# Kernel optimization log

Measured on AMD Instinct MI355X. Metric: run time of the kernel, lower is better.

Reference implementation:

```python
import jax, jax.numpy as jnp
import numpy as np

B, P, NEG = 1024, 10, 990
NU, NI = 10000, 20000
MOMENTUM = 0.9
EPS = 1e-10
FAIR_W = 100000.0


def setup_inputs() -> dict:
    key = jax.random.key(0)
    k1, k2, k3, k4, k5, k6 = jax.random.split(key, 6)
    predictions = jax.random.normal(k1, (B, P + NEG), dtype=jnp.float32)
    stats = jax.random.uniform(k2, (NU + 1, NI + 1), dtype=jnp.float32) * 0.1
    user_id = jax.random.randint(k3, (B,), 0, NU + 1)
    item_id = jax.random.randint(k4, (B, P), 0, NI + 1)
    # binary group indicator masks (float, as they multiply the softmax)
    a_index = (jax.random.uniform(k5, (B, P + NEG)) < 0.5).astype(jnp.float32)
    b_index = (jax.random.uniform(k6, (B, P + NEG)) < 0.5).astype(jnp.float32)
    return {"predictions": predictions, "stats": stats, "user_id": user_id,
            "item_id": item_id, "a_index": a_index, "b_index": b_index}


def reference(predictions, stats, user_id, item_id, a_index, b_index):
    batch_size = predictions.shape[0]
    # (batch pos) 1  and  (batch pos) neg
    pos = predictions[:, :P].reshape(batch_size * P, 1)
    neg = jnp.repeat(predictions[:, P:], P, axis=0)          # [(B*P), NEG]
    score_margins = neg - pos                                 # [(B*P), NEG]
    exp_margins = jax.lax.stop_gradient(
        jnp.exp(score_margins - jnp.max(score_margins)))
    user_rep = jnp.repeat(user_id, P)                         # [(B*P)]
    pos_items = item_id[:, :P].reshape(-1)                    # [(B*P)]
    exp_margin_means = jnp.mean(exp_margins, axis=1)
    current = stats[user_rep, pos_items]                      # gather
    updated = (1.0 - MOMENTUM) * current + MOMENTUM * exp_margin_means
    new_stats = stats.at[user_rep, pos_items].set(updated)    # scatter
    normalized = jax.lax.stop_gradient(exp_margins / (updated[:, None] + EPS))
    main_loss = jnp.sum(score_margins * normalized) / batch_size
    # fairness term (expectation_mode='1' -> unit expectation weights)
    psm = jax.nn.softmax(predictions, axis=1)
    a_exp = jnp.sum(a_index * psm, axis=1)
    b_exp = jnp.sum(b_index * psm, axis=1)
    diff = b_exp - a_exp
    fw_sqrt = np.sqrt(FAIR_W).astype(np.float32)
    fairness = (diff * fw_sqrt) ** 2                          # balanced
    loss = main_loss + jnp.mean(fairness)
    return loss, new_stats
```

## Files before the change

### kernel.cpp

```cpp
#include <hip/hip_runtime.h>
#include <math.h>

constexpr int kB    = 1024;
constexpr int kP    = 10;
constexpr int kNeg  = 990;
constexpr int kCols = 1000;
constexpr int kNI1  = 20001;
constexpr long long kStatsN = 200030001LL;
constexpr float kMom = 0.9f;
constexpr float kEps = 1e-10f;

constexpr int kOffT0   = 0;
constexpr int kOffT1   = 1024;
constexpr int kOffMM   = 2048;
constexpr int kOffFair = 3072;
constexpr int kOffM    = 4096;
constexpr int kOffFS   = 4097;
constexpr int kOffAcc  = 4098;
constexpr int kOffUpd  = 4100;
constexpr int kOffKey  = 14340;

__device__ inline float wave_sum(float v) {
    for (int o = 32; o > 0; o >>= 1) v += __shfl_xor(v, o, 64);
    return v;
}
__device__ inline float wave_max(float v) {
    for (int o = 32; o > 0; o >>= 1) v = fmaxf(v, __shfl_xor(v, o, 64));
    return v;
}
__device__ inline float wave_min(float v) {
    for (int o = 32; o > 0; o >>= 1) v = fminf(v, __shfl_xor(v, o, 64));
    return v;
}

__global__ __launch_bounds__(256) void k_rowstats(const float* __restrict__ pred,
                                                  const float* __restrict__ aidx,
                                                  const float* __restrict__ bidx,
                                                  float* __restrict__ ws) {
    const int b = blockIdx.x;
    const int t = threadIdx.x;
    const float* row = pred + (long long)b * kCols;
    const float* ar  = aidx + (long long)b * kCols;
    const float* br  = bidx + (long long)b * kCols;

    float sumexp = 0.f, sa = 0.f, sb = 0.f, T0 = 0.f, T1 = 0.f;
    float posmin = INFINITY, negmax = -INFINITY;
#pragma unroll
    for (int q = 0; q < 4; ++q) {
        int i = t + q * 256;
        if (i < kCols) {
            float x  = row[i];
            float ex = expf(x);
            sumexp += ex;
            sa += ar[i] * ex;
            sb += br[i] * ex;
            if (i < kP) {
                posmin = fminf(posmin, x);
            } else {
                negmax = fmaxf(negmax, x);
                T0 += ex;
                T1 += x * ex;
            }
        }
    }
    sumexp = wave_sum(sumexp);
    sa     = wave_sum(sa);
    sb     = wave_sum(sb);
    T0     = wave_sum(T0);
    T1     = wave_sum(T1);
    posmin = wave_min(posmin);
    negmax = wave_max(negmax);

    __shared__ float red[7][4];
    const int w = t >> 6, lane = t & 63;
    if (lane == 0) {
        red[0][w] = sumexp; red[1][w] = sa; red[2][w] = sb;
        red[3][w] = T0;     red[4][w] = T1;
        red[5][w] = posmin; red[6][w] = negmax;
    }
    __syncthreads();
    if (t == 0) {
        float se = 0.f, a = 0.f, bb = 0.f, t0 = 0.f, t1 = 0.f;
        float pm = INFINITY, nm = -INFINITY;
#pragma unroll
        for (int i = 0; i < 4; ++i) {
            se += red[0][i]; a += red[1][i]; bb += red[2][i];
            t0 += red[3][i]; t1 += red[4][i];
            pm = fminf(pm, red[5][i]); nm = fmaxf(nm, red[6][i]);
        }
        float diff = (bb - a) / se;
        float fw   = sqrtf(100000.0f);
        float d2   = diff * fw;
        ws[kOffT0 + b]   = t0;
        ws[kOffT1 + b]   = t1;
        ws[kOffMM + b]   = nm - pm;
        ws[kOffFair + b] = d2 * d2;
    }
}

__global__ __launch_bounds__(256) void k_reduce(float* __restrict__ ws) {
    const int t = threadIdx.x;
    float mm = -INFINITY, fs = 0.f;
#pragma unroll
    for (int q = 0; q < 4; ++q) {
        int i = t + q * 256;
        mm = fmaxf(mm, ws[kOffMM + i]);
        fs += ws[kOffFair + i];
    }
    mm = wave_max(mm);
    fs = wave_sum(fs);
    __shared__ float rm[4], rs[4];
    const int w = t >> 6, lane = t & 63;
    if (lane == 0) { rm[w] = mm; rs[w] = fs; }
    __syncthreads();
    if (t == 0) {
        float M = fmaxf(fmaxf(rm[0], rm[1]), fmaxf(rm[2], rm[3]));
        float F = rs[0] + rs[1] + rs[2] + rs[3];
        ws[kOffM]   = M;
        ws[kOffFS]  = F;
        ws[kOffAcc] = 0.f;
    }
}

__global__ __launch_bounds__(256) void k_perk(const float* __restrict__ pred,
                                              const float* __restrict__ stats,
                                              const int* __restrict__ uid,
                                              const int* __restrict__ iid,
                                              float* __restrict__ ws) {
    const int k = blockIdx.x * 256 + threadIdx.x;
    const float M = ws[kOffM];
    const int b = k / kP;
    const int p = k - b * kP;
    float pos = pred[(long long)b * kCols + p];
    float T0  = ws[kOffT0 + b];
    float T1  = ws[kOffT1 + b];
    float s   = expf(-pos - M);
    float mean_e = s * T0 * (1.0f / kNeg);
    int u  = uid[b];
    int it = iid[k];
    int key = u * kNI1 + it;
    float cur = stats[(long long)key];
    float upd = (1.0f - kMom) * cur + kMom * mean_e;
    ws[kOffUpd + k] = upd;
    ((int*)ws)[kOffKey + k] = key;
    float c = s * (T1 - pos * T0) / (upd + kEps);

    c = wave_sum(c);
    __shared__ float rs[4];
    const int w = threadIdx.x >> 6, lane = threadIdx.x & 63;
    if (lane == 0) rs[w] = c;
    __syncthreads();
    if (threadIdx.x == 0) {
        atomicAdd(&ws[kOffAcc], rs[0] + rs[1] + rs[2] + rs[3]);
    }
}

__global__ __launch_bounds__(256) void k_copy(const float* __restrict__ src,
                                              float* __restrict__ dst) {
    const long long base = (long long)blockIdx.x * 1024 + threadIdx.x;
#pragma unroll
    for (int q = 0; q < 4; ++q) {
        long long i = base + (long long)q * 256;
        if (i < kStatsN) dst[i] = src[i];
    }
}

__global__ __launch_bounds__(256) void k_scatter(float* __restrict__ out,
                                                 const float* __restrict__ ws) {
    const int k = blockIdx.x;
    const int* keys = (const int*)ws + kOffKey;
    __shared__ int dupflag;
    if (threadIdx.x == 0) dupflag = 0;
    __syncthreads();
    const int key = keys[k];
    for (int j = k + 1 + threadIdx.x; j < kB * kP; j += 256) {
        if (keys[j] == key) dupflag = 1;
    }
    __syncthreads();
    if (threadIdx.x == 0 && !dupflag) {
        out[1 + (long long)key] = ws[kOffUpd + k];
    }
    if (blockIdx.x == 0 && threadIdx.x == 255) {
        out[0] = ws[kOffAcc] * (1.0f / kB) + ws[kOffFS] * (1.0f / kB);
    }
}

extern "C" void kernel_launch(void* const* d_in, const int* in_sizes, int n_in,
                              void* d_out, int out_size, void* d_ws, size_t ws_size,
                              hipStream_t stream) {
    const float* pred  = (const float*)d_in[0];
    const float* stats = (const float*)d_in[1];
    const int*   uid   = (const int*)d_in[2];
    const int*   iid   = (const int*)d_in[3];
    const float* aidx  = (const float*)d_in[4];
    const float* bidx  = (const float*)d_in[5];
    float* out = (float*)d_out;
    float* ws  = (float*)d_ws;

    k_rowstats<<<kB, 256, 0, stream>>>(pred, aidx, bidx, ws);
    k_reduce<<<1, 256, 0, stream>>>(ws);
    k_perk<<<(kB * kP) / 256, 256, 0, stream>>>(pred, stats, uid, iid, ws);
    long long nblocks = (kStatsN + 1023) / 1024;
    k_copy<<<(int)nblocks, 256, 0, stream>>>(stats, out + 1);
    k_scatter<<<kB * kP, 256, 0, stream>>>(out, ws);
}
```

Measured before the change: 1.315 ms.

## Fuse stats copy into rowstats kernel and fold global reduce into perk

Merges the row-statistics kernel and the stats copy into one launch, with extra blocks that copy the stats table. Because the output is offset by one float, each block does float4 loads and shifts lanes so its stores are aligned, and a few edge elements are written separately. The separate single-block reduce kernel is removed: every perk block recomputes the global max margin, and block 0 writes the fairness sum. This saves launches and makes the large copy vectorised, at the cost of redundant reductions and two float4 loads per copied chunk.

After: 1.272 ms. 3.3% less time.

```diff
diff --git a/kernel.cpp b/kernel.cpp
--- a/kernel.cpp
+++ b/kernel.cpp
@@ -14,12 +14,16 @@
 constexpr int kOffT1   = 1024;
 constexpr int kOffMM   = 2048;
 constexpr int kOffFair = 3072;
-constexpr int kOffM    = 4096;
 constexpr int kOffFS   = 4097;
 constexpr int kOffAcc  = 4098;
 constexpr int kOffUpd  = 4100;
 constexpr int kOffKey  = 14340;
 
+constexpr long long kChunks = (kStatsN - 3) / 4;
+constexpr int kChunksPerBlock = 1024;
+constexpr int kCopyBlocks =
+    (int)((kChunks + kChunksPerBlock - 1) / kChunksPerBlock);
+
 __device__ inline float wave_sum(float v) {
     for (int o = 32; o > 0; o >>= 1) v += __shfl_xor(v, o, 64);
     return v;
@@ -33,92 +37,99 @@
     return v;
 }
 
-__global__ __launch_bounds__(256) void k_rowstats(const float* __restrict__ pred,
-                                                  const float* __restrict__ aidx,
-                                                  const float* __restrict__ bidx,
-                                                  float* __restrict__ ws) {
-    const int b = blockIdx.x;
+__global__ __launch_bounds__(256) void k_main(const float* __restrict__ pred,
+                                              const float* __restrict__ aidx,
+                                              const float* __restrict__ bidx,
+                                              const float* __restrict__ stats,
+                                              float* __restrict__ out,
+                                              float* __restrict__ ws) {
+    const int blk = blockIdx.x;
     const int t = threadIdx.x;
-    const float* row = pred + (long long)b * kCols;
-    const float* ar  = aidx + (long long)b * kCols;
-    const float* br  = bidx + (long long)b * kCols;
-
-    float sumexp = 0.f, sa = 0.f, sb = 0.f, T0 = 0.f, T1 = 0.f;
-    float posmin = INFINITY, negmax = -INFINITY;
+
+    if (blk < kB) {
+        if (blk == 0) {
+            if (t == 64) {
+                out[1] = stats[0]; out[2] = stats[1]; out[3] = stats[2];
+            } else if (t == 65) {
+                out[kStatsN - 1] = stats[kStatsN - 2];
+                out[kStatsN]     = stats[kStatsN - 1];
+            } else if (t == 66) {
+                ws[kOffAcc] = 0.f;
+            }
+        }
+        const int b = blk;
+        const float* row = pred + (long long)b * kCols;
+        const float* ar  = aidx + (long long)b * kCols;
+        const float* br  = bidx + (long long)b * kCols;
+
+        float sumexp = 0.f, sa = 0.f, sb = 0.f, T0 = 0.f, T1 = 0.f;
+        float posmin = INFINITY, negmax = -INFINITY;
+#pragma unroll
+        for (int q = 0; q < 4; ++q) {
+            int i = t + q * 256;
+            if (i < kCols) {
+                float x  = row[i];
+                float ex = expf(x);
+                sumexp += ex;
+                sa += ar[i] * ex;
+                sb += br[i] * ex;
+                if (i < kP) {
+                    posmin = fminf(posmin, x);
+                } else {
+                    negmax = fmaxf(negmax, x);
+                    T0 += ex;
+                    T1 += x * ex;
+                }
+            }
+        }
+        sumexp = wave_sum(sumexp);
+        sa     = wave_sum(sa);
+        sb     = wave_sum(sb);
+        T0     = wave_sum(T0);
+        T1     = wave_sum(T1);
+        posmin = wave_min(posmin);
+        negmax = wave_max(negmax);
+
+        __shared__ float red[7][4];
+        const int w = t >> 6, lane = t & 63;
+        if (lane == 0) {
+            red[0][w] = sumexp; red[1][w] = sa; red[2][w] = sb;
+            red[3][w] = T0;     red[4][w] = T1;
+            red[5][w] = posmin; red[6][w] = negmax;
+        }
+        __syncthreads();
+        if (t == 0) {
+            float se = 0.f, a = 0.f, bb = 0.f, t0 = 0.f, t1 = 0.f;
+            float pm = INFINITY, nm = -INFINITY;
+#pragma unroll
+            for (int i = 0; i < 4; ++i) {
+                se += red[0][i]; a += red[1][i]; bb += red[2][i];
+                t0 += red[3][i]; t1 += red[4][i];
+                pm = fminf(pm, red[5][i]); nm = fmaxf(nm, red[6][i]);
+            }
+            float diff = (bb - a) / se;
+            float fw   = sqrtf(100000.0f);
+            float d2   = diff * fw;
+            ws[kOffT0 + b]   = t0;
+            ws[kOffT1 + b]   = t1;
+            ws[kOffMM + b]   = nm - pm;
+            ws[kOffFair + b] = d2 * d2;
+        }
+        return;
+    }
+
+    const long long c0 = (long long)(blk - kB) * kChunksPerBlock + t;
+    const float4* __restrict__ s4 = (const float4*)stats;
 #pragma unroll
     for (int q = 0; q < 4; ++q) {
-        int i = t + q * 256;
-        if (i < kCols) {
-            float x  = row[i];
-            float ex = expf(x);
-            sumexp += ex;
-            sa += ar[i] * ex;
-            sb += br[i] * ex;
-            if (i < kP) {
-                posmin = fminf(posmin, x);
-            } else {
-                negmax = fmaxf(negmax, x);
-                T0 += ex;
-                T1 += x * ex;
-            }
-        }
-    }
-    sumexp = wave_sum(sumexp);
-    sa     = wave_sum(sa);
-    sb     = wave_sum(sb);
-    T0     = wave_sum(T0);
-    T1     = wave_sum(T1);
-    posmin = wave_min(posmin);
-    negmax = wave_max(negmax);
-
-    __shared__ float red[7][4];
-    const int w = t >> 6, lane = t & 63;
-    if (lane == 0) {
-        red[0][w] = sumexp; red[1][w] = sa; red[2][w] = sb;
-        red[3][w] = T0;     red[4][w] = T1;
-        red[5][w] = posmin; red[6][w] = negmax;
-    }
-    __syncthreads();
-    if (t == 0) {
-        float se = 0.f, a = 0.f, bb = 0.f, t0 = 0.f, t1 = 0.f;
-        float pm = INFINITY, nm = -INFINITY;
-#pragma unroll
-        for (int i = 0; i < 4; ++i) {
-            se += red[0][i]; a += red[1][i]; bb += red[2][i];
-            t0 += red[3][i]; t1 += red[4][i];
-            pm = fminf(pm, red[5][i]); nm = fmaxf(nm, red[6][i]);
-        }
-        float diff = (bb - a) / se;
-        float fw   = sqrtf(100000.0f);
-        float d2   = diff * fw;
-        ws[kOffT0 + b]   = t0;
-        ws[kOffT1 + b]   = t1;
-        ws[kOffMM + b]   = nm - pm;
-        ws[kOffFair + b] = d2 * d2;
-    }
-}
-
-__global__ __launch_bounds__(256) void k_reduce(float* __restrict__ ws) {
-    const int t = threadIdx.x;
-    float mm = -INFINITY, fs = 0.f;
-#pragma unroll
-    for (int q = 0; q < 4; ++q) {
-        int i = t + q * 256;
-        mm = fmaxf(mm, ws[kOffMM + i]);
-        fs += ws[kOffFair + i];
-    }
-    mm = wave_max(mm);
-    fs = wave_sum(fs);
-    __shared__ float rm[4], rs[4];
-    const int w = t >> 6, lane = t & 63;
-    if (lane == 0) { rm[w] = mm; rs[w] = fs; }
-    __syncthreads();
-    if (t == 0) {
-        float M = fmaxf(fmaxf(rm[0], rm[1]), fmaxf(rm[2], rm[3]));
-        float F = rs[0] + rs[1] + rs[2] + rs[3];
-        ws[kOffM]   = M;
-        ws[kOffFS]  = F;
-        ws[kOffAcc] = 0.f;
+        long long c = c0 + (long long)q * 256;
+        if (c < kChunks) {
+            float4 A  = s4[c];
+            float4 Bv = s4[c + 1];
+            float4 r;
+            r.x = A.w; r.y = Bv.x; r.z = Bv.y; r.w = Bv.z;
+            *reinterpret_cast<float4*>(out + 4 + 4 * c) = r;
+        }
     }
 }
 
@@ -127,8 +138,33 @@
                                               const int* __restrict__ uid,
                                               const int* __restrict__ iid,
                                               float* __restrict__ ws) {
-    const int k = blockIdx.x * 256 + threadIdx.x;
-    const float M = ws[kOffM];
+    const int t = threadIdx.x;
+    const int w = t >> 6, lane = t & 63;
+
+    float mm = -INFINITY;
+#pragma unroll
+    for (int q = 0; q < 4; ++q) mm = fmaxf(mm, ws[kOffMM + t + q * 256]);
+    mm = wave_max(mm);
+
+    float fs = 0.f;
+    if (blockIdx.x == 0) {
+#pragma unroll
+        for (int q = 0; q < 4; ++q) fs += ws[kOffFair + t + q * 256];
+        fs = wave_sum(fs);
+    }
+
+    __shared__ float rm[4], rf[4];
+    __shared__ float Msh;
+    if (lane == 0) { rm[w] = mm; if (blockIdx.x == 0) rf[w] = fs; }
+    __syncthreads();
+    if (t == 0) {
+        Msh = fmaxf(fmaxf(rm[0], rm[1]), fmaxf(rm[2], rm[3]));
+        if (blockIdx.x == 0) ws[kOffFS] = rf[0] + rf[1] + rf[2] + rf[3];
+    }
+    __syncthreads();
+    const float M = Msh;
+
+    const int k = blockIdx.x * 256 + t;
     const int b = k / kP;
     const int p = k - b * kP;
     float pos = pred[(long long)b * kCols + p];
@@ -146,22 +182,11 @@
     float c = s * (T1 - pos * T0) / (upd + kEps);
 
     c = wave_sum(c);
-    __shared__ float rs[4];
-    const int w = threadIdx.x >> 6, lane = threadIdx.x & 63;
-    if (lane == 0) rs[w] = c;
-    __syncthreads();
-    if (threadIdx.x == 0) {
-        atomicAdd(&ws[kOffAcc], rs[0] + rs[1] + rs[2] + rs[3]);
-    }
-}
-
-__global__ __launch_bounds__(256) void k_copy(const float* __restrict__ src,
-                                              float* __restrict__ dst) {
-    const long long base = (long long)blockIdx.x * 1024 + threadIdx.x;
-#pragma unroll
-    for (int q = 0; q < 4; ++q) {
-        long long i = base + (long long)q * 256;
-        if (i < kStatsN) dst[i] = src[i];
+    __shared__ float racc[4];
+    if (lane == 0) racc[w] = c;
+    __syncthreads();
+    if (t == 0) {
+        atomicAdd(&ws[kOffAcc], racc[0] + racc[1] + racc[2] + racc[3]);
     }
 }
 
@@ -197,10 +222,7 @@
     float* out = (float*)d_out;
     float* ws  = (float*)d_ws;
 
-    k_rowstats<<<kB, 256, 0, stream>>>(pred, aidx, bidx, ws);
-    k_reduce<<<1, 256, 0, stream>>>(ws);
+    k_main<<<kB + kCopyBlocks, 256, 0, stream>>>(pred, aidx, bidx, stats, out, ws);
     k_perk<<<(kB * kP) / 256, 256, 0, stream>>>(pred, stats, uid, iid, ws);
-    long long nblocks = (kStatsN + 1023) / 1024;
-    k_copy<<<(int)nblocks, 256, 0, stream>>>(stats, out + 1);
     k_scatter<<<kB * kP, 256, 0, stream>>>(out, ws);
 }
```
